# Performance work log

Measured on AMD Instinct MI355X. Metric: run time of the kernel, lower is better.

The kernel has to match this reference:

```python
import jax, jax.numpy as jnp
import numpy as np

CLIP_LIMIT = 4.0
GRID = (8, 8)
NBINS = 256
B, H, W = 8, 2048, 2048


def setup_inputs() -> dict:
    key = jax.random.key(0)
    img = jax.random.randint(key, (B, H, W), 0, 256).astype(jnp.float32)
    return {"image": img}


def _clahe(image):
    b, h, w = image.shape
    gy, gx = GRID
    th, tw = h // gy, w // gx
    area = th * tw
    # quantize to bins (indices are non-differentiable constants)
    bins = jnp.clip(jax.lax.stop_gradient(image), 0, 255).astype(jnp.int32)  # [B,H,W]

    # ---- per-tile 256-bin histograms via scatter-add ----
    tiles = bins.reshape(b, gy, th, gx, tw).transpose(0, 1, 3, 2, 4)
    tiles = tiles.reshape(b * gy * gx, area)                       # [ntiles, area]
    n = b * gy * gx
    hist = jnp.zeros((n, NBINS), jnp.int32).at[jnp.arange(n)[:, None], tiles].add(1)

    # ---- clip and redistribute excess (OpenCV semantics) ----
    clip_lim = max(int(CLIP_LIMIT * area / NBINS), 1)
    clipped = jnp.minimum(hist, clip_lim)
    excess = (hist - clipped).sum(-1)                              # [ntiles]
    clipped = clipped + (excess // NBINS)[:, None]
    residual = excess % NBINS
    step = jnp.maximum(NBINS // jnp.maximum(residual, 1), 1)       # [ntiles]
    i = jnp.arange(NBINS)
    clipped = clipped + jnp.where(
        (residual[:, None] > 0) & (i[None, :] % step[:, None] == 0), 1, 0)

    # ---- CDF -> per-tile LUT ----
    cdf = jnp.cumsum(clipped, axis=-1)
    lut = jnp.clip(jnp.round(cdf.astype(jnp.float32) * (255.0 / area)), 0.0, 255.0)
    lut = lut.reshape(b, gy, gx, NBINS)                            # [B,gy,gx,256]

    # ---- bilinear interpolation between the 4 neighboring tile LUTs ----
    yf = jnp.arange(h, dtype=jnp.float32) / th - 0.5
    xf = jnp.arange(w, dtype=jnp.float32) / tw - 0.5
    y1f, x1f = jnp.floor(yf), jnp.floor(xf)
    ya, xa = yf - y1f, xf - x1f                                    # frac weights
    y1 = jnp.clip(y1f.astype(jnp.int32), 0, gy - 1)
    y2 = jnp.clip(y1f.astype(jnp.int32) + 1, 0, gy - 1)
    x1 = jnp.clip(x1f.astype(jnp.int32), 0, gx - 1)
    x2 = jnp.clip(x1f.astype(jnp.int32) + 1, 0, gx - 1)

    bi = jnp.arange(b)[:, None, None]        # [B,1,1]
    Y1, Y2 = y1[None, :, None], y2[None, :, None]   # [1,H,1]
    X1, X2 = x1[None, None, :], x2[None, None, :]   # [1,1,W]
    l11 = lut[bi, Y1, X1, bins]
    l12 = lut[bi, Y1, X2, bins]
    l21 = lut[bi, Y2, X1, bins]
    l22 = lut[bi, Y2, X2, bins]

    wy = ya[None, :, None]
    wx = xa[None, None, :]
    res = (l11 * (1 - wx) + l12 * wx) * (1 - wy) + (l21 * (1 - wx) + l22 * wx) * wy
    return jnp.clip(jnp.round(res), 0.0, 255.0)


def reference(image) -> jnp.ndarray:
    return _clahe(image)
```

## Files before the change

### kernel.cpp

```cpp
#include <hip/hip_runtime.h>

#define NB 256
#define CLIP_LIM 1024
#define HSTRIDE 264
#define NSUB 32
#define PSTRIDE 9

typedef float f32x4 __attribute__((ext_vector_type(4)));

__global__ __launch_bounds__(1024, 8) void clahe_hist_lut(const float* __restrict__ img,
                                                          float* __restrict__ lut,
                                                          unsigned int* __restrict__ bins) {
    const int t   = blockIdx.x;
    const int b   = t >> 6;
    const int ty  = (t >> 3) & 7;
    const int tx  = t & 7;
    const int tid = threadIdx.x;
    const int sub = ((tid >> 6) << 1) | (tid & 1);

    __shared__ int h[NSUB * HSTRIDE];
    __shared__ int c[NB];
    __shared__ int s_excess;

    #pragma unroll
    for (int k = 0; k < 9; ++k) {
        const int idx = tid + k * 1024;
        if (idx < NSUB * HSTRIDE) h[idx] = 0;
    }
    if (tid == 0) s_excess = 0;
    __syncthreads();

    const float* base = img + ((size_t)b << 22) + (size_t)(ty * 256) * 2048 + tx * 256;
    unsigned int* bbase = bins + ((size_t)b << 20) + ty * 131072 + tx * 64;
    int* hw = &h[sub * HSTRIDE];

    for (int i = tid; i < 16384; i += 1024) {
        const int r = i >> 6;
        const int q = i & 63;
        const f32x4 v = *reinterpret_cast<const f32x4*>(base + (size_t)r * 2048 + q * 4);
        const int b0 = (int)fminf(fmaxf(v.x, 0.f), 255.f);
        const int b1 = (int)fminf(fmaxf(v.y, 0.f), 255.f);
        const int b2 = (int)fminf(fmaxf(v.z, 0.f), 255.f);
        const int b3 = (int)fminf(fmaxf(v.w, 0.f), 255.f);
        atomicAdd(&hw[b0], 1);
        atomicAdd(&hw[b1], 1);
        atomicAdd(&hw[b2], 1);
        atomicAdd(&hw[b3], 1);
        bbase[r * 512 + q] = (unsigned)b0 | ((unsigned)b1 << 8) |
                             ((unsigned)b2 << 16) | ((unsigned)b3 << 24);
    }
    __syncthreads();

    int clipped = 0;
    if (tid < NB) {
        int sum = 0;
        #pragma unroll
        for (int w = 0; w < NSUB; ++w) sum += h[w * HSTRIDE + tid];
        clipped = min(sum, CLIP_LIM);
        atomicAdd(&s_excess, sum - clipped);
    }
    __syncthreads();

    if (tid < NB) {
        const int excess   = s_excess;
        const int add      = excess >> 8;
        const int residual = excess & 255;
        int step = 256 / (residual > 0 ? residual : 1);
        if (step < 1) step = 1;
        c[tid] = clipped + add + ((residual > 0 && (tid % step) == 0) ? 1 : 0);
    }
    __syncthreads();

    #pragma unroll
    for (int off = 1; off < NB; off <<= 1) {
        int v = 0;
        if (tid < NB && tid >= off) v = c[tid - off];
        __syncthreads();
        if (tid < NB) c[tid] += v;
        __syncthreads();
    }

    if (tid < NB) {
        float lv = rintf((float)c[tid] * (255.0f / 65536.0f));
        lut[t * NB + tid] = fminf(fmaxf(lv, 0.f), 255.f);
    }
}

__global__ __launch_bounds__(256, 8) void clahe_apply(const unsigned int* __restrict__ bins,
                                                      const float* __restrict__ lut,
                                                      float* __restrict__ out) {
    const int bi  = blockIdx.x;
    const int b   = bi >> 10;
    const int y0  = (bi & 1023) * 2;
    const int tid = threadIdx.x;

    __shared__ unsigned int T[2 * NB * PSTRIDE];

    {
        const float yf  = (float)y0 * (1.0f / 256.0f) - 0.5f;
        const float y1f = floorf(yf);
        const int y1 = min(max((int)y1f, 0), 7);
        const int y2 = min(max((int)y1f + 1, 0), 7);
        const float* lb = lut + ((size_t)b << 14);
        float la[8], lc[8];
        #pragma unroll
        for (int xc = 0; xc < 8; ++xc) {
            la[xc] = lb[(y1 * 8 + xc) * NB + tid];
            lc[xc] = lb[(y2 * 8 + xc) * NB + tid];
        }
        #pragma unroll
        for (int r = 0; r < 2; ++r) {
            const float q = (float)((y0 + r + 128) & 255);
            float tv[10];
            #pragma unroll
            for (int k = 0; k < 10; ++k) {
                const int kc = (k == 0) ? 0 : ((k - 1 > 7) ? 7 : k - 1);
                tv[k] = la[kc] * (256.0f - q) + lc[kc] * q;
            }
            unsigned int* Tr = &T[r * NB * PSTRIDE + tid * PSTRIDE];
            #pragma unroll
            for (int s = 0; s < 9; ++s)
                Tr[s] = (unsigned int)tv[s] | ((unsigned int)tv[s + 1] << 16);
        }
    }
    __syncthreads();

    const size_t imgbase = ((size_t)b << 22) + (size_t)y0 * 2048;
    #pragma unroll
    for (int it = 0; it < 4; ++it) {
        const int r = it >> 1;
        const int i = (it & 1) * 256 + tid;
        const size_t prow = imgbase + (size_t)r * 2048;
        const unsigned int w = bins[(prow >> 2) + i];
        const unsigned int* Tr = &T[r * NB * PSTRIDE];
        const int x   = i * 4;
        const int s   = (x + 128) >> 8;
        const float xa0 = (float)((x + 128) & 255);
        float res[4];
        #pragma unroll
        for (int j = 0; j < 4; ++j) {
            const int bn = (w >> (8 * j)) & 255;
            const unsigned int u = Tr[bn * PSTRIDE + s];
            const float a  = (float)(u & 0xFFFFu);
            const float bb = (float)(u >> 16);
            const float xa = (xa0 + (float)j) * (1.0f / 256.0f);
            const float v  = a + (bb - a) * xa;
            res[j] = fminf(fmaxf(rintf(v * (1.0f / 256.0f)), 0.f), 255.f);
        }
        const f32x4 o = { res[0], res[1], res[2], res[3] };
        __builtin_nontemporal_store(o, reinterpret_cast<f32x4*>(out + prow + i * 4));
    }
}

extern "C" void kernel_launch(void* const* d_in, const int* in_sizes, int n_in,
                              void* d_out, int out_size, void* d_ws, size_t ws_size,
                              hipStream_t stream) {
    const float* img = (const float*)d_in[0];
    float* out = (float*)d_out;
    float* lut = (float*)d_ws;
    unsigned int* bins = (unsigned int*)((char*)d_ws + 512 * 1024);

    clahe_hist_lut<<<512, 1024, 0, stream>>>(img, lut, bins);
    clahe_apply<<<8 * 1024, 256, 0, stream>>>(bins, lut, out);
}
```

Before: 78.33 us.

## Split histogram into row-band partials plus separate LUT reduction kernel

```diff
diff --git a/kernel.cpp b/kernel.cpp
--- a/kernel.cpp
+++ b/kernel.cpp
@@ -3,41 +3,34 @@
 #define NB 256
 #define CLIP_LIM 1024
 #define HSTRIDE 264
-#define NSUB 32
 #define PSTRIDE 9
 
 typedef float f32x4 __attribute__((ext_vector_type(4)));
 
-__global__ __launch_bounds__(1024, 8) void clahe_hist_lut(const float* __restrict__ img,
-                                                          float* __restrict__ lut,
-                                                          unsigned int* __restrict__ bins) {
-    const int t   = blockIdx.x;
-    const int b   = t >> 6;
-    const int ty  = (t >> 3) & 7;
-    const int tx  = t & 7;
-    const int tid = threadIdx.x;
-    const int sub = ((tid >> 6) << 1) | (tid & 1);
+__global__ __launch_bounds__(1024) void clahe_hist(const float* __restrict__ img,
+                                                   unsigned int* __restrict__ bins,
+                                                   unsigned int* __restrict__ part) {
+    const int blk  = blockIdx.x;
+    const int tid  = threadIdx.x;
+    const int sub  = ((tid >> 6) << 1) | (tid & 1);
 
-    __shared__ int h[NSUB * HSTRIDE];
-    __shared__ int c[NB];
-    __shared__ int s_excess;
+    __shared__ int h[32 * HSTRIDE];
 
     #pragma unroll
     for (int k = 0; k < 9; ++k) {
         const int idx = tid + k * 1024;
-        if (idx < NSUB * HSTRIDE) h[idx] = 0;
+        if (idx < 32 * HSTRIDE) h[idx] = 0;
     }
-    if (tid == 0) s_excess = 0;
     __syncthreads();
 
-    const float* base = img + ((size_t)b << 22) + (size_t)(ty * 256) * 2048 + tx * 256;
-    unsigned int* bbase = bins + ((size_t)b << 20) + ty * 131072 + tx * 64;
+    const size_t B0 = (size_t)blk * 16384;
     int* hw = &h[sub * HSTRIDE];
 
-    for (int i = tid; i < 16384; i += 1024) {
-        const int r = i >> 6;
-        const int q = i & 63;
-        const f32x4 v = *reinterpret_cast<const f32x4*>(base + (size_t)r * 2048 + q * 4);
+    #pragma unroll
+    for (int k = 0; k < 16; ++k) {
+        const size_t g = B0 + k * 1024 + tid;
+        const f32x4 v = __builtin_nontemporal_load(
+            reinterpret_cast<const f32x4*>(img + g * 4));
         const int b0 = (int)fminf(fmaxf(v.x, 0.f), 255.f);
         const int b1 = (int)fminf(fmaxf(v.y, 0.f), 255.f);
         const int b2 = (int)fminf(fmaxf(v.z, 0.f), 255.f);
@@ -46,44 +39,60 @@
         atomicAdd(&hw[b1], 1);
         atomicAdd(&hw[b2], 1);
         atomicAdd(&hw[b3], 1);
-        bbase[r * 512 + q] = (unsigned)b0 | ((unsigned)b1 << 8) |
-                             ((unsigned)b2 << 16) | ((unsigned)b3 << 24);
-    }
-    __syncthreads();
-
-    int clipped = 0;
-    if (tid < NB) {
-        int sum = 0;
-        #pragma unroll
-        for (int w = 0; w < NSUB; ++w) sum += h[w * HSTRIDE + tid];
-        clipped = min(sum, CLIP_LIM);
-        atomicAdd(&s_excess, sum - clipped);
-    }
-    __syncthreads();
-
-    if (tid < NB) {
-        const int excess   = s_excess;
-        const int add      = excess >> 8;
-        const int residual = excess & 255;
-        int step = 256 / (residual > 0 ? residual : 1);
-        if (step < 1) step = 1;
-        c[tid] = clipped + add + ((residual > 0 && (tid % step) == 0) ? 1 : 0);
+        bins[g] = (unsigned)b0 | ((unsigned)b1 << 8) |
+                  ((unsigned)b2 << 16) | ((unsigned)b3 << 24);
     }
     __syncthreads();
 
     #pragma unroll
+    for (int e = tid; e < 2048; e += 1024) {
+        const int tx = e >> 8;
+        const int bn = e & 255;
+        const int s = h[(2 * tx) * HSTRIDE + bn] + h[(2 * tx + 1) * HSTRIDE + bn] +
+                      h[(2 * tx + 16) * HSTRIDE + bn] + h[(2 * tx + 17) * HSTRIDE + bn];
+        part[(size_t)blk * 2048 + e] = (unsigned int)s;
+    }
+}
+
+__global__ __launch_bounds__(256) void clahe_lut(const unsigned int* __restrict__ part,
+                                                 float* __restrict__ lut) {
+    const int t    = blockIdx.x;
+    const int band = t >> 3;
+    const int tx   = t & 7;
+    const int tid  = threadIdx.x;
+
+    __shared__ int c[NB];
+    __shared__ int s_excess;
+    if (tid == 0) s_excess = 0;
+    __syncthreads();
+
+    int sum = 0;
+    #pragma unroll
+    for (int j = 0; j < 8; ++j)
+        sum += (int)part[(size_t)(band * 8 + j) * 2048 + tx * 256 + tid];
+
+    const int clipped0 = min(sum, CLIP_LIM);
+    atomicAdd(&s_excess, sum - clipped0);
+    __syncthreads();
+
+    const int excess   = s_excess;
+    const int add      = excess >> 8;
+    const int residual = excess & 255;
+    int step = 256 / (residual > 0 ? residual : 1);
+    if (step < 1) step = 1;
+    c[tid] = clipped0 + add + ((residual > 0 && (tid % step) == 0) ? 1 : 0);
+    __syncthreads();
+
+    #pragma unroll
     for (int off = 1; off < NB; off <<= 1) {
-        int v = 0;
-        if (tid < NB && tid >= off) v = c[tid - off];
+        const int v = (tid >= off) ? c[tid - off] : 0;
         __syncthreads();
-        if (tid < NB) c[tid] += v;
+        c[tid] += v;
         __syncthreads();
     }
 
-    if (tid < NB) {
-        float lv = rintf((float)c[tid] * (255.0f / 65536.0f));
-        lut[t * NB + tid] = fminf(fmaxf(lv, 0.f), 255.f);
-    }
+    float lv = rintf((float)c[tid] * (255.0f / 65536.0f));
+    lut[t * NB + tid] = fminf(fmaxf(lv, 0.f), 255.f);
 }
 
 __global__ __launch_bounds__(256, 8) void clahe_apply(const unsigned int* __restrict__ bins,
@@ -159,7 +168,9 @@
     float* out = (float*)d_out;
     float* lut = (float*)d_ws;
     unsigned int* bins = (unsigned int*)((char*)d_ws + 512 * 1024);
+    unsigned int* part = (unsigned int*)((char*)d_ws + 512 * 1024 + 33554432);
 
-    clahe_hist_lut<<<512, 1024, 0, stream>>>(img, lut, bins);
+    clahe_hist<<<512, 1024, 0, stream>>>(img, bins, part);
+    clahe_lut<<<512, 256, 0, stream>>>(part, lut);
     clahe_apply<<<8 * 1024, 256, 0, stream>>>(bins, lut, out);
 }
```

New measurement: 68.06 us. -13.1%, faster.
